# Performance work log

Measured on AMD Instinct MI355X. Metric: run time of the kernel, lower is better.

Reference implementation:

```python
import jax, jax.numpy as jnp
import numpy as np

B, C, L = 256, 256, 512
EPS = 1e-5

def setup_inputs() -> dict:
    key = jax.random.key(0)
    k1, k2, k3, k4 = jax.random.split(key, 4)
    x = jax.random.normal(k1, (B, C, L), dtype=jnp.float32)
    idx = jax.random.randint(k2, (B, L), 0, L + 1, dtype=jnp.int32)  # L == pad slot
    # Conv1d(2C, C, 1): weight [C, 2C], bias [C]
    W = jax.random.normal(k3, (C, 2 * C), dtype=jnp.float32) * (1.0 / np.sqrt(2 * C))
    b = jax.random.normal(k4, (C,), dtype=jnp.float32) * 0.01
    return {"x": x, "idx": idx, "W": W, "b": b}

def reference(x, idx, W, b):
    # collect_neighbours: pad length dim with one zero column, gather per (b, l)
    x_pad = jnp.pad(x, ((0, 0), (0, 0), (0, 1)))            # [B, C, L+1]
    nbr = jnp.take_along_axis(x_pad, idx[:, None, :].astype(jnp.int32), axis=2)  # [B, C, L]
    cat = jnp.concatenate([x, nbr], axis=1)                 # [B, 2C, L]
    # 1x1 Conv1d == channel matmul
    y = jnp.einsum('oc,bcl->bol', W, cat) + b[None, :, None]  # [B, C, L]
    # InstanceNorm1d (affine=False): normalize over L per (b, c), biased var
    mu = jnp.mean(y, axis=2, keepdims=True)
    var = jnp.mean(jnp.square(y - mu), axis=2, keepdims=True)
    y = (y - mu) * jax.lax.rsqrt(var + EPS)
    return jax.nn.relu(y)
```

## Files before the change

kernel.cpp:

```cpp
#include <hip/hip_runtime.h>
#include <hip/hip_bf16.h>
#include <stdint.h>

typedef __bf16 bf16x8 __attribute__((ext_vector_type(8)));
typedef float  f32x4  __attribute__((ext_vector_type(4)));

__device__ __forceinline__ uint32_t cvt2(float a, float b) {
    __hip_bfloat162 h = __float22bfloat162_rn(make_float2(a, b));
    uint32_t u; __builtin_memcpy(&u, &h, 4); return u;
}
__device__ __forceinline__ float bflo(uint32_t u) { uint32_t t = u << 16;         float f; __builtin_memcpy(&f, &t, 4); return f; }
__device__ __forceinline__ float bfhi(uint32_t u) { uint32_t t = u & 0xffff0000u; float f; __builtin_memcpy(&f, &t, 4); return f; }
__device__ __forceinline__ int swz(int u) { return u ^ ((u >> 3) & 7); }

__global__ __launch_bounds__(256, 2)
void edgeconv_fused(const float* __restrict__ x,
                    const int*   __restrict__ idx,
                    const float* __restrict__ W,
                    float*       __restrict__ out)
{
    __shared__ __align__(16) unsigned char smem[65536];
    unsigned short* wlds = (unsigned short*)smem;
    unsigned short* xT   = (unsigned short*)(smem + 32768);
    unsigned short* y2   = (unsigned short*)smem;
    float*          red  = (float*)(smem + 38912);

    const int tid  = threadIdx.x;
    const int wv   = tid >> 6;
    const int lane = tid & 63;
    const int m    = lane & 15;
    const int q    = lane >> 4;

    const int id  = blockIdx.x;
    const int rem = id & 63;
    const int b   = ((id >> 6) << 3) + (rem & 7);
    const int o0  = (rem >> 3) << 5;

    const float* xb = x + ((size_t)b << 17);

    #pragma unroll
    for (int i = 0; i < 16; ++i) {
        int r = (i << 2) + wv;
        const float4 f = *(const float4*)(W + ((size_t)(o0 + (r & 31)) << 9)
                                            + ((r >> 5) << 8) + (lane << 2));
        uint2 p; p.x = cvt2(f.x, f.y); p.y = cvt2(f.z, f.w);
        int sl = lane >> 1;
        *(uint2*)(wlds + (sl << 9) + ((swz(r) ^ (sl & 7)) << 3) + ((lane & 1) << 2)) = p;
    }

    f32x4 acc[4][8];
    #pragma unroll
    for (int mt = 0; mt < 4; ++mt)
        #pragma unroll
        for (int nt = 0; nt < 8; ++nt)
            acc[mt][nt] = (f32x4){0.f, 0.f, 0.f, 0.f};

    float4 xr0[8], xr1[8];
    auto loadg = [&](int kc, int g, float4* xr) {
        int gid = (g << 8) + tid;
        int s2  = gid >> 7;
        int l4  = gid & 127;
        const float* base = xb + ((size_t)((kc << 5) + (s2 << 3)) << 9) + (l4 << 2);
        #pragma unroll
        for (int j = 0; j < 8; ++j) xr[j] = *(const float4*)(base + (j << 9));
    };
    auto storeg = [&](int g, const float4* xr) {
        int gid = (g << 8) + tid;
        int s2  = gid >> 7;
        int l4  = gid & 127;
        #pragma unroll
        for (int lv = 0; lv < 4; ++lv) {
            int l = (l4 << 2) + lv;
            uint4 p;
            p.x = cvt2((&xr[0].x)[lv], (&xr[1].x)[lv]);
            p.y = cvt2((&xr[2].x)[lv], (&xr[3].x)[lv]);
            p.z = cvt2((&xr[4].x)[lv], (&xr[5].x)[lv]);
            p.w = cvt2((&xr[6].x)[lv], (&xr[7].x)[lv]);
            *(uint4*)(xT + (s2 << 12) + (swz(l) << 3)) = p;
        }
    };

    loadg(0, 0, xr0);
    loadg(0, 1, xr1);
    storeg(0, xr0);
    storeg(1, xr1);
    __syncthreads();

    for (int kc = 0; kc < 8; ++kc) {
        if (kc < 7) loadg(kc + 1, 0, xr0);

        bf16x8 av[4], bv[8];
        #pragma unroll
        for (int mt = 0; mt < 4; ++mt) {
            int sl = (kc << 2) + q;
            av[mt] = *(const bf16x8*)(wlds + (sl << 9) + ((swz((mt << 4) + m) ^ (sl & 7)) << 3));
        }
        #pragma unroll
        for (int nt = 0; nt < 8; ++nt)
            bv[nt] = *(const bf16x8*)(xT + (q << 12) + (swz((wv << 7) + (nt << 4) + m) << 3));

        #pragma unroll
        for (int mt = 0; mt < 4; ++mt)
            #pragma unroll
            for (int nt = 0; nt < 8; ++nt)
                acc[mt][nt] = __builtin_amdgcn_mfma_f32_16x16x32_bf16(av[mt], bv[nt], acc[mt][nt], 0, 0, 0);

        if (kc < 7) loadg(kc + 1, 1, xr1);
        __syncthreads();
        if (kc < 7) {
            storeg(0, xr0);
            storeg(1, xr1);
            __syncthreads();
        }
    }

    int iv[8];
    #pragma unroll
    for (int nt = 0; nt < 8; ++nt)
        iv[nt] = idx[((size_t)b << 9) + (wv << 7) + (nt << 4) + m];

    #pragma unroll
    for (int mt = 2; mt < 4; ++mt)
        #pragma unroll
        for (int nt = 0; nt < 8; ++nt) {
            int col  = (wv << 7) + (nt << 4) + m;
            int row0 = ((mt - 2) << 4) + (q << 2);
            uint2 p;
            p.x = cvt2(acc[mt][nt][0], acc[mt][nt][1]);
            p.y = cvt2(acc[mt][nt][2], acc[mt][nt][3]);
            *(uint2*)(y2 + col * 36 + row0) = p;
        }
    __syncthreads();

    float vvl[2][8][4];
    float s_[2][4], q_[2][4];
    #pragma unroll
    for (int mt = 0; mt < 2; ++mt)
        #pragma unroll
        for (int r4 = 0; r4 < 4; ++r4) { s_[mt][r4] = 0.f; q_[mt][r4] = 0.f; }

    #pragma unroll
    for (int nt = 0; nt < 8; ++nt) {
        int  c   = iv[nt];
        bool inb = (c < 512);
        int  cc  = inb ? c : 0;
        #pragma unroll
        for (int mt = 0; mt < 2; ++mt) {
            uint2 g = *(const uint2*)(y2 + cc * 36 + (mt << 4) + (q << 2));
            float gv[4];
            gv[0] = inb ? bflo(g.x) : 0.f;
            gv[1] = inb ? bfhi(g.x) : 0.f;
            gv[2] = inb ? bflo(g.y) : 0.f;
            gv[3] = inb ? bfhi(g.y) : 0.f;
            #pragma unroll
            for (int r4 = 0; r4 < 4; ++r4) {
                float val = acc[mt][nt][r4] + gv[r4];
                vvl[mt][nt][r4] = val;
                s_[mt][r4] += val;
                q_[mt][r4] += val * val;
            }
        }
    }

    #pragma unroll
    for (int mt = 0; mt < 2; ++mt)
        #pragma unroll
        for (int r4 = 0; r4 < 4; ++r4) {
            float s = s_[mt][r4], ss = q_[mt][r4];
            #pragma unroll
            for (int off = 1; off < 16; off <<= 1) {
                s  += __shfl_xor(s,  off, 64);
                ss += __shfl_xor(ss, off, 64);
            }
            if (m == 0) {
                int r = (mt << 4) + (q << 2) + r4;
                red[(r << 3) + (wv << 1)]     = s;
                red[(r << 3) + (wv << 1) + 1] = ss;
            }
        }
    __syncthreads();

    #pragma unroll
    for (int mt = 0; mt < 2; ++mt)
        #pragma unroll
        for (int r4 = 0; r4 < 4; ++r4) {
            int r = (mt << 4) + (q << 2) + r4;
            float S = red[(r << 3)]     + red[(r << 3) + 2] + red[(r << 3) + 4] + red[(r << 3) + 6];
            float Q = red[(r << 3) + 1] + red[(r << 3) + 3] + red[(r << 3) + 5] + red[(r << 3) + 7];
            float mu  = S * (1.0f / 512.0f);
            float var = Q * (1.0f / 512.0f) - mu * mu;
            float rs  = rsqrtf(var + 1e-5f);
            float* op = out + (((size_t)(b << 8) + o0 + r) << 9) + (wv << 7) + m;
            #pragma unroll
            for (int nt = 0; nt < 8; ++nt) {
                float t = (vvl[mt][nt][r4] - mu) * rs;
                op[nt << 4] = fmaxf(t, 0.0f);
            }
        }
}

extern "C" void kernel_launch(void* const* d_in, const int* in_sizes, int n_in,
                              void* d_out, int out_size, void* d_ws, size_t ws_size,
                              hipStream_t stream) {
    const float* x   = (const float*)d_in[0];
    const int*   idx = (const int*)  d_in[1];
    const float* W   = (const float*)d_in[2];
    float* out = (float*)d_out;

    edgeconv_fused<<<dim3(2048), dim3(256), 0, stream>>>(x, idx, W, out);
}
```

Measured before the change: 317.2 us.

## Split into bf16 pack-transpose prepass and LDS-free GEMM with fused norm

Adds a prepass kernel that converts x and W to bf16 once, in an MFMA-friendly transposed layout in workspace. The GEMM kernel then reads operands straight from global memory, with no LDS staging or in-loop syncs. Before, each x tile was converted eight times (once per output-channel group). The cost is an extra kernel launch plus a 64 MB bf16 round trip through global memory. The old fused kernel is kept as a fallback when the workspace is too small.

```diff
diff --git a/kernel.cpp b/kernel.cpp
--- a/kernel.cpp
+++ b/kernel.cpp
@@ -12,6 +12,187 @@
 __device__ __forceinline__ float bflo(uint32_t u) { uint32_t t = u << 16;         float f; __builtin_memcpy(&f, &t, 4); return f; }
 __device__ __forceinline__ float bfhi(uint32_t u) { uint32_t t = u & 0xffff0000u; float f; __builtin_memcpy(&f, &t, 4); return f; }
 __device__ __forceinline__ int swz(int u) { return u ^ ((u >> 3) & 7); }
+
+__global__ __launch_bounds__(256, 4)
+void pack_transpose(const float* __restrict__ x, const float* __restrict__ W,
+                    unsigned short* __restrict__ xT, unsigned short* __restrict__ wT)
+{
+    const int tid = threadIdx.x;
+    const int id  = blockIdx.x;
+    if (id < 2048) {
+        const int b = id >> 3, kc = id & 7;
+        const int s2 = tid >> 6, l4 = tid & 63;
+        const float* src0 = x + ((size_t)b << 17) + ((size_t)((kc << 5) + (s2 << 3)) << 9);
+        unsigned short* dst0 = xT + (((size_t)(b << 5) + (kc << 2) + s2) << 12);
+        #pragma unroll
+        for (int lh = 0; lh < 2; ++lh) {
+            const int l0 = (lh << 8) + (l4 << 2);
+            float4 xr[8];
+            #pragma unroll
+            for (int j = 0; j < 8; ++j)
+                xr[j] = *(const float4*)(src0 + (j << 9) + l0);
+            #pragma unroll
+            for (int lv = 0; lv < 4; ++lv) {
+                uint4 p;
+                p.x = cvt2((&xr[0].x)[lv], (&xr[1].x)[lv]);
+                p.y = cvt2((&xr[2].x)[lv], (&xr[3].x)[lv]);
+                p.z = cvt2((&xr[4].x)[lv], (&xr[5].x)[lv]);
+                p.w = cvt2((&xr[6].x)[lv], (&xr[7].x)[lv]);
+                *(uint4*)(dst0 + ((l0 + lv) << 3)) = p;
+            }
+        }
+    } else {
+        const int og = id - 2048;
+        const int r = tid & 63, sg = tid >> 6;
+        const float* wrow = W + ((size_t)((og << 5) + (r & 31)) << 9) + ((r >> 5) << 8);
+        #pragma unroll
+        for (int ss = 0; ss < 8; ++ss) {
+            const int s = (sg << 3) + ss;
+            float4 f0 = *(const float4*)(wrow + (s << 3));
+            float4 f1 = *(const float4*)(wrow + (s << 3) + 4);
+            uint4 p;
+            p.x = cvt2(f0.x, f0.y); p.y = cvt2(f0.z, f0.w);
+            p.z = cvt2(f1.x, f1.y); p.w = cvt2(f1.z, f1.w);
+            *(uint4*)(wT + (((((og << 5) + s) << 6) + r) << 3)) = p;
+        }
+    }
+}
+
+__global__ __launch_bounds__(256, 2)
+void edge_gemm(const unsigned short* __restrict__ xT,
+               const unsigned short* __restrict__ wT,
+               const int* __restrict__ idx,
+               float* __restrict__ out)
+{
+    __shared__ __align__(16) unsigned char smem[37888];
+    unsigned short* y2 = (unsigned short*)smem;
+    float* red         = (float*)(smem + 36864);
+
+    const int tid  = threadIdx.x;
+    const int wv   = tid >> 6;
+    const int lane = tid & 63;
+    const int m    = lane & 15;
+    const int q    = lane >> 4;
+
+    const int id  = blockIdx.x;
+    const int rem = id & 63;
+    const int b   = ((id >> 6) << 3) + (rem & 7);
+    const int og  = rem >> 3;
+    const int o0  = og << 5;
+
+    const unsigned short* xb = xT + ((size_t)b << 17);
+    const unsigned short* wb = wT + (og << 14);
+
+    int iv[8];
+    #pragma unroll
+    for (int nt = 0; nt < 8; ++nt)
+        iv[nt] = idx[((size_t)b << 9) + (wv << 7) + (nt << 4) + m];
+
+    f32x4 acc[4][8];
+    #pragma unroll
+    for (int mt = 0; mt < 4; ++mt)
+        #pragma unroll
+        for (int nt = 0; nt < 8; ++nt)
+            acc[mt][nt] = (f32x4){0.f, 0.f, 0.f, 0.f};
+
+    #pragma unroll
+    for (int kc = 0; kc < 8; ++kc) {
+        const int s = (kc << 2) + q;
+        bf16x8 av[4], bv[8];
+        const unsigned short* ab = wb + (s << 9) + (m << 3);
+        #pragma unroll
+        for (int mt = 0; mt < 4; ++mt)
+            av[mt] = *(const bf16x8*)(ab + (mt << 7));
+        const unsigned short* bb = xb + (s << 12) + (((wv << 7) + m) << 3);
+        #pragma unroll
+        for (int nt = 0; nt < 8; ++nt)
+            bv[nt] = *(const bf16x8*)(bb + (nt << 7));
+        #pragma unroll
+        for (int mt = 0; mt < 4; ++mt)
+            #pragma unroll
+            for (int nt = 0; nt < 8; ++nt)
+                acc[mt][nt] = __builtin_amdgcn_mfma_f32_16x16x32_bf16(av[mt], bv[nt], acc[mt][nt], 0, 0, 0);
+    }
+
+    #pragma unroll
+    for (int mt = 2; mt < 4; ++mt)
+        #pragma unroll
+        for (int nt = 0; nt < 8; ++nt) {
+            int col  = (wv << 7) + (nt << 4) + m;
+            int row0 = ((mt - 2) << 4) + (q << 2);
+            uint2 p;
+            p.x = cvt2(acc[mt][nt][0], acc[mt][nt][1]);
+            p.y = cvt2(acc[mt][nt][2], acc[mt][nt][3]);
+            *(uint2*)(y2 + col * 36 + row0) = p;
+        }
+    __syncthreads();
+
+    float vvl[2][8][4];
+    float s_[2][4], q_[2][4];
+    #pragma unroll
+    for (int mt = 0; mt < 2; ++mt)
+        #pragma unroll
+        for (int r4 = 0; r4 < 4; ++r4) { s_[mt][r4] = 0.f; q_[mt][r4] = 0.f; }
+
+    #pragma unroll
+    for (int nt = 0; nt < 8; ++nt) {
+        int  c   = iv[nt];
+        bool inb = (c < 512);
+        int  cc  = inb ? c : 0;
+        #pragma unroll
+        for (int mt = 0; mt < 2; ++mt) {
+            uint2 g = *(const uint2*)(y2 + cc * 36 + (mt << 4) + (q << 2));
+            float gv[4];
+            gv[0] = inb ? bflo(g.x) : 0.f;
+            gv[1] = inb ? bfhi(g.x) : 0.f;
+            gv[2] = inb ? bflo(g.y) : 0.f;
+            gv[3] = inb ? bfhi(g.y) : 0.f;
+            #pragma unroll
+            for (int r4 = 0; r4 < 4; ++r4) {
+                float val = acc[mt][nt][r4] + gv[r4];
+                vvl[mt][nt][r4] = val;
+                s_[mt][r4] += val;
+                q_[mt][r4] += val * val;
+            }
+        }
+    }
+
+    #pragma unroll
+    for (int mt = 0; mt < 2; ++mt)
+        #pragma unroll
+        for (int r4 = 0; r4 < 4; ++r4) {
+            float s = s_[mt][r4], ss = q_[mt][r4];
+            #pragma unroll
+            for (int off = 1; off < 16; off <<= 1) {
+                s  += __shfl_xor(s,  off, 64);
+                ss += __shfl_xor(ss, off, 64);
+            }
+            if (m == 0) {
+                int r = (mt << 4) + (q << 2) + r4;
+                red[(r << 3) + (wv << 1)]     = s;
+                red[(r << 3) + (wv << 1) + 1] = ss;
+            }
+        }
+    __syncthreads();
+
+    #pragma unroll
+    for (int mt = 0; mt < 2; ++mt)
+        #pragma unroll
+        for (int r4 = 0; r4 < 4; ++r4) {
+            int r = (mt << 4) + (q << 2) + r4;
+            float S = red[(r << 3)]     + red[(r << 3) + 2] + red[(r << 3) + 4] + red[(r << 3) + 6];
+            float Q = red[(r << 3) + 1] + red[(r << 3) + 3] + red[(r << 3) + 5] + red[(r << 3) + 7];
+            float mu  = S * (1.0f / 512.0f);
+            float var = Q * (1.0f / 512.0f) - mu * mu;
+            float rs  = rsqrtf(var + 1e-5f);
+            float* op = out + (((size_t)(b << 8) + o0 + r) << 9) + (wv << 7) + m;
+            #pragma unroll
+            for (int nt = 0; nt < 8; ++nt) {
+                float t = (vvl[mt][nt][r4] - mu) * rs;
+                op[nt << 4] = fmaxf(t, 0.0f);
+            }
+        }
+}
 
 __global__ __launch_bounds__(256, 2)
 void edgeconv_fused(const float* __restrict__ x,
@@ -207,5 +388,15 @@
     const float* W   = (const float*)d_in[2];
     float* out = (float*)d_out;
 
-    edgeconv_fused<<<dim3(2048), dim3(256), 0, stream>>>(x, idx, W, out);
+    const size_t xT_bytes = (size_t)256 * 32 * 512 * 8 * 2;
+    const size_t wT_bytes = (size_t)8 * 32 * 64 * 8 * 2;
+
+    if (ws_size >= xT_bytes + wT_bytes) {
+        unsigned short* xT = (unsigned short*)d_ws;
+        unsigned short* wT = (unsigned short*)((char*)d_ws + xT_bytes);
+        pack_transpose<<<dim3(2056), dim3(256), 0, stream>>>(x, W, xT, wT);
+        edge_gemm<<<dim3(2048), dim3(256), 0, stream>>>(xT, wT, idx, out);
+    } else {
+        edgeconv_fused<<<dim3(2048), dim3(256), 0, stream>>>(x, idx, W, out);
+    }
 }
```

After: 303.5 us. 1.05x faster.
